# Performance work log

Hardware: AMD Instinct MI355X
Metric: run time of the kernel (lower is better)

## Reference

```python
import jax, jax.numpy as jnp
import numpy as np

H = 2048       # hidden_size
NH = 16        # num query heads
NKV = 4        # num key/value heads
HD = 128       # head_dim
EPS = 1e-6
ROPE_BASE = 10000.0


def rms_norm(x, w):
    xf = x.astype(jnp.float32)
    var = jnp.mean(xf * xf, axis=-1, keepdims=True)
    return (w * (xf * jax.lax.rsqrt(var + EPS)).astype(x.dtype))


def rope_cos_sin(seq_len, dtype):
    inv_freq = 1.0 / (ROPE_BASE ** (jnp.arange(0, HD, 2, dtype=jnp.float32) / HD))
    pos = jnp.arange(seq_len, dtype=jnp.float32)
    ang = pos[:, None] * inv_freq[None, :]            # [S, HD/2]
    emb = jnp.concatenate([ang, ang], axis=-1)        # [S, HD]
    return jnp.cos(emb).astype(dtype), jnp.sin(emb).astype(dtype)


def rotate_half(x):
    x1, x2 = jnp.split(x, 2, axis=-1)
    return jnp.concatenate([-x2, x1], axis=-1)


def setup_inputs() -> dict:
    key = jax.random.key(0)
    ks = jax.random.split(key, 8)
    B, S = 2, 2048
    hidden_states = jax.random.normal(ks[0], (B, S, H), dtype=jnp.float32)
    # additive causal mask [B,1,S,S]
    causal = jnp.where(jnp.tril(jnp.ones((S, S), dtype=bool)), 0.0, -1e9).astype(jnp.float32)
    attention_mask = jnp.broadcast_to(causal[None, None], (B, 1, S, S))
    sc = 1.0 / np.sqrt(H)
    Wq = jax.random.normal(ks[1], (NH * HD, H), dtype=jnp.float32) * sc
    Wk = jax.random.normal(ks[2], (NKV * HD, H), dtype=jnp.float32) * sc
    Wv = jax.random.normal(ks[3], (NKV * HD, H), dtype=jnp.float32) * sc
    Wo = jax.random.normal(ks[4], (H, NH * HD), dtype=jnp.float32) * sc
    q_norm_w = jnp.ones((HD,), dtype=jnp.float32)
    k_norm_w = jnp.ones((HD,), dtype=jnp.float32)
    return {"hidden_states": hidden_states, "attention_mask": attention_mask,
            "Wq": Wq, "Wk": Wk, "Wv": Wv, "Wo": Wo,
            "q_norm_w": q_norm_w, "k_norm_w": k_norm_w}


def reference(hidden_states, attention_mask, Wq, Wk, Wv, Wo, q_norm_w, k_norm_w):
    B, S, _ = hidden_states.shape
    # projections (nn.Linear: x @ W.T)
    q = (hidden_states @ Wq.T).reshape(B, S, NH, HD).transpose(0, 2, 1, 3)   # [B,NH,S,HD]
    k = (hidden_states @ Wk.T).reshape(B, S, NKV, HD).transpose(0, 2, 1, 3)  # [B,NKV,S,HD]
    v = (hidden_states @ Wv.T).reshape(B, S, NKV, HD).transpose(0, 2, 1, 3)
    # QK RMSNorm over head_dim
    q = rms_norm(q, q_norm_w)
    k = rms_norm(k, k_norm_w)
    # RoPE
    cos, sin = rope_cos_sin(S, q.dtype)        # [S,HD]
    q = q * cos + rotate_half(q) * sin
    k = k * cos + rotate_half(k) * sin
    # GQA: repeat kv heads
    n_rep = NH // NKV
    k = jnp.repeat(k, n_rep, axis=1)           # [B,NH,S,HD]
    v = jnp.repeat(v, n_rep, axis=1)
    # attention
    scores = jnp.einsum('bhqd,bhkd->bhqk', q, k) / np.sqrt(HD)
    scores = scores + attention_mask
    probs = jax.nn.softmax(scores, axis=-1)
    attn = jnp.einsum('bhqk,bhkd->bhqd', probs, v)
    attn = attn.transpose(0, 2, 1, 3).reshape(B, S, NH * HD)
    return attn @ Wo.T
```

## Files before the change

### kernel.cpp

```cpp
#include <hip/hip_runtime.h>
#include <hip/hip_bf16.h>
#include <math.h>

#define NH 16
#define NKV 4
#define HD 128
#define SEQ 2048
#define BATCH 2
#define EPSF 1e-6f
#define QKV 3072

typedef __attribute__((ext_vector_type(8))) short bf16x8;
typedef __attribute__((ext_vector_type(4))) short short4v;
typedef __attribute__((ext_vector_type(4))) float f32x4;

__device__ __forceinline__ short f2bf(float x) {
    unsigned u = __float_as_uint(x);
    u += 0x7fffu + ((u >> 16) & 1u);
    return (short)(u >> 16);
}
__device__ __forceinline__ float bf2f(short x) {
    return __uint_as_float((unsigned)(unsigned short)x << 16);
}
__device__ __forceinline__ unsigned pkbf(float a, float b) {
    __hip_bfloat162 h = __float22bfloat162_rn(float2{a, b});
    unsigned r; __builtin_memcpy(&r, &h, 4); return r;
}

__device__ __forceinline__ void gll16(const short* g, short* l) {
    __builtin_amdgcn_global_load_lds(
        (const __attribute__((address_space(1))) unsigned*)g,
        (__attribute__((address_space(3))) unsigned*)l, 16, 0, 0);
}

__global__ __launch_bounds__(256)
void cast_all(const float* __restrict__ hs, const float* __restrict__ Wq,
              const float* __restrict__ Wk, const float* __restrict__ Wv,
              const float* __restrict__ Wo, short* __restrict__ hsb,
              short* __restrict__ wqkv, short* __restrict__ wob)
{
    const size_t MEG = 1024 * 1024;
    const int id = blockIdx.x;
    const float* s;
    short* d;
    size_t off;
    if (id < 8192)       { s = hs; d = hsb;            off = (size_t)id * 1024; }
    else if (id < 12288) { s = Wq; d = wqkv;           off = (size_t)(id - 8192) * 1024; }
    else if (id < 13312) { s = Wk; d = wqkv + 4 * MEG; off = (size_t)(id - 12288) * 1024; }
    else if (id < 14336) { s = Wv; d = wqkv + 5 * MEG; off = (size_t)(id - 13312) * 1024; }
    else                 { s = Wo; d = wob;            off = (size_t)(id - 14336) * 1024; }
    const size_t i = off + threadIdx.x * 4;
    float4 v = *(const float4*)(s + i);
    short4v o;
    o.x = f2bf(v.x); o.y = f2bf(v.y); o.z = f2bf(v.z); o.w = f2bf(v.w);
    *(short4v*)(d + i) = o;
}

template<bool OUT_BF16>
__global__ __launch_bounds__(256, 3)
void gemm_nt_mfma(const short* __restrict__ A, const short* __restrict__ B,
                  void* __restrict__ Cv, int N, int K, int gridX, int total)
{
    __shared__ short As[128 * 64];
    __shared__ short Bs[128 * 64];

    const int tid = threadIdx.x;
    const int w = tid >> 6, lane = tid & 63;
    const int quad = lane >> 4, ln = lane & 15;
    const int mw = (w >> 1) * 64, nw = (w & 1) * 64;

    const int id = blockIdx.x;
    const int t = (id & 7) * (total >> 3) + (id >> 3);
    const int n0 = (t % gridX) * 128;
    const int m0 = (t / gridX) * 128;

    const int rr = lane >> 3;
    const int gsw = ((lane & 7) ^ rr) * 8;
    const short* Ag[4]; const short* Bg[4];
    short* Al[4]; short* Bl[4];
    #pragma unroll
    for (int r = 0; r < 4; ++r) {
        const int row = w * 8 + 32 * r + rr;
        Ag[r] = A + (size_t)(m0 + row) * K + gsw;
        Bg[r] = B + (size_t)(n0 + row) * K + gsw;
        Al[r] = &As[(w * 8 + 32 * r) * 64];
        Bl[r] = &Bs[(w * 8 + 32 * r) * 64];
    }

    const int col0 = ((quad) ^ (ln & 7)) * 8;
    const int col1 = ((4 + quad) ^ (ln & 7)) * 8;

    f32x4 acc[4][4];
    #pragma unroll
    for (int i = 0; i < 4; ++i)
        #pragma unroll
        for (int j = 0; j < 4; ++j)
            acc[i][j] = (f32x4){0.f, 0.f, 0.f, 0.f};

    for (int k0 = 0; k0 < K; k0 += 64) {
        __syncthreads();
        #pragma unroll
        for (int r = 0; r < 4; ++r) {
            gll16(Ag[r] + k0, Al[r]);
            gll16(Bg[r] + k0, Bl[r]);
        }
        __syncthreads();

        #pragma unroll
        for (int ks = 0; ks < 2; ++ks) {
            const int col = ks ? col1 : col0;
            bf16x8 af[4], bfr[4];
            #pragma unroll
            for (int i = 0; i < 4; ++i)
                af[i] = *(const bf16x8*)&As[(mw + i * 16 + ln) * 64 + col];
            #pragma unroll
            for (int j = 0; j < 4; ++j)
                bfr[j] = *(const bf16x8*)&Bs[(nw + j * 16 + ln) * 64 + col];
            #pragma unroll
            for (int i = 0; i < 4; ++i)
                #pragma unroll
                for (int j = 0; j < 4; ++j)
                    acc[i][j] = __builtin_amdgcn_mfma_f32_16x16x32_bf16(
                        af[i], bfr[j], acc[i][j], 0, 0, 0);
        }
    }

    #pragma unroll
    for (int i = 0; i < 4; ++i) {
        #pragma unroll
        for (int reg = 0; reg < 4; ++reg) {
            const int row = m0 + mw + i * 16 + quad * 4 + reg;
            const size_t base = (size_t)row * N + n0 + nw;
            #pragma unroll
            for (int j = 0; j < 4; ++j) {
                if (OUT_BF16)
                    ((short*)Cv)[base + j * 16 + ln] = f2bf(acc[i][j][reg]);
                else
                    ((float*)Cv)[base + j * 16 + ln] = acc[i][j][reg];
            }
        }
    }
}

__global__ __launch_bounds__(256)
void norm_rope_bf16(short* __restrict__ qkv, const float* __restrict__ qw,
                    const float* __restrict__ kw)
{
    const int wave = threadIdx.x >> 6;
    const int lane = threadIdx.x & 63;
    const long vec = (long)blockIdx.x * 4 + wave;
    const long NQ = (long)BATCH * SEQ * NH;

    short* base;
    const float* w;
    int s;
    if (vec < NQ) {
        const long token = vec / NH;
        const int h = (int)(vec % NH);
        s = (int)(token % SEQ);
        base = qkv + token * QKV + h * HD;
        w = qw;
    } else {
        const long t = vec - NQ;
        const long token = t / NKV;
        const int kvh = (int)(t % NKV);
        s = (int)(token % SEQ);
        base = qkv + token * QKV + 2048 + kvh * HD;
        w = kw;
    }

    float x0 = bf2f(base[lane]);
    float x1 = bf2f(base[lane + 64]);
    float ss = x0 * x0 + x1 * x1;
    #pragma unroll
    for (int off = 32; off; off >>= 1) ss += __shfl_xor(ss, off, 64);
    const float r = rsqrtf(ss * (1.0f / HD) + EPSF);
    x0 = x0 * r * w[lane];
    x1 = x1 * r * w[lane + 64];

    const float inv_freq = expf(-(float)lane * (logf(10000.0f) / 64.0f));
    const float ang = (float)s * inv_freq;
    const float c = cosf(ang);
    const float sn = sinf(ang);
    base[lane]      = f2bf(x0 * c - x1 * sn);
    base[lane + 64] = f2bf(x1 * c + x0 * sn);
}

__global__ __launch_bounds__(256)
void transpose_v(const short* __restrict__ qkv, short* __restrict__ vT)
{
    __shared__ short T[32][33];
    const int bx = blockIdx.x;
    const int st = bx & 63;
    const int dt = (bx >> 6) & 3;
    const int bk = bx >> 8;
    const int s0 = st * 32, d0 = dt * 32;
    const int tid = threadIdx.x;
    const long tok0 = (long)(bk >> 2) * SEQ + s0;
    const int kvh = bk & 3;

    const int rs = tid >> 3;
    const int rc = (tid & 7) * 4;
    short4v val = *(const short4v*)(qkv + (tok0 + rs) * QKV + 2560 + kvh * HD + d0 + rc);
    T[rc + 0][rs] = val.x; T[rc + 1][rs] = val.y;
    T[rc + 2][rs] = val.z; T[rc + 3][rs] = val.w;
    __syncthreads();

    const int wd = tid >> 3;
    const int wsc = (tid & 7) * 4;
    short4v ov;
    ov.x = T[wd][wsc + 0]; ov.y = T[wd][wsc + 1];
    ov.z = T[wd][wsc + 2]; ov.w = T[wd][wsc + 3];
    *(short4v*)(vT + ((size_t)bk * HD + d0 + wd) * SEQ + s0 + wsc) = ov;
}

__global__ __launch_bounds__(512, 4)
void flash_attn_mfma(const short* __restrict__ qkv, const short* __restrict__ vT,
                     short* __restrict__ o)
{
    __shared__ short Ks[64][144];
    __shared__ short Vt[128][80];
    __shared__ short Ps[8][16][80];

    const int tid = threadIdx.x;
    const int w = tid >> 6;
    const int lane = tid & 63;
    const int quad = lane >> 4;
    const int ln = lane & 15;
    const int side = w >> 2;
    const int sw = w & 3;

    const int bx = blockIdx.x;
    const int pair = bx & 15;
    const int bh = bx >> 4;
    const int h = bh & 15;
    const int b = bh >> 4;
    const int kvh = h >> 2;
    const int qa = pair, qb = 31 - pair;
    const int qX = side ? qb : qa;
    const int rX = qX * 64 + sw * 16;

    const float SC = 0.08838834764831845f * 1.4426950408889634f;

    bf16x8 qf[4];
    {
        const short* qrow = qkv + (size_t)(b * SEQ + rX + ln) * QKV + h * HD;
        #pragma unroll
        for (int f = 0; f < 4; ++f)
            qf[f] = *(const bf16x8*)(qrow + f * 32 + quad * 8);
    }

    f32x4 Oa[8];
    #pragma unroll
    for (int dg = 0; dg < 8; ++dg) Oa[dg] = (f32x4){0.f, 0.f, 0.f, 0.f};
    float mX = -1e30f, lX = 0.f;

    const short* kbase = qkv + (size_t)(b * SEQ) * QKV + 2048 + kvh * HD;
    const short* vbase = vT + (size_t)(b * NKV + kvh) * HD * SEQ;

    bf16x8 kp[2], vp[2];
    auto prefetch = [&](int k0) {
        #pragma unroll
        for (int i = 0; i < 2; ++i) {
            const int e = tid + i * 512;
            kp[i] = *(const bf16x8*)(kbase + (size_t)(k0 + (e >> 4)) * QKV + (e & 15) * 8);
            vp[i] = *(const bf16x8*)(vbase + (size_t)(e >> 3) * SEQ + k0 + (e & 7) * 8);
        }
    };
    prefetch(0);

    for (int kt = 0; kt <= qb; ++kt) {
        const int k0 = kt * 64;
        __syncthreads();
        #pragma unroll
        for (int i = 0; i < 2; ++i) {
            const int e = tid + i * 512;
            *(bf16x8*)&Ks[e >> 4][(e & 15) * 8] = kp[i];
            *(bf16x8*)&Vt[e >> 3][(e & 7) * 8] = vp[i];
        }
        __syncthreads();
        if (kt < qb) prefetch(k0 + 64);

        if (kt <= qX) {
            f32x4 s[4];
            #pragma unroll
            for (int g = 0; g < 4; ++g) {
                f32x4 acc = (f32x4){0.f, 0.f, 0.f, 0.f};
                #pragma unroll
                for (int f = 0; f < 4; ++f) {
                    bf16x8 kf = *(const bf16x8*)&Ks[g * 16 + ln][f * 32 + quad * 8];
                    acc = __builtin_amdgcn_mfma_f32_16x16x32_bf16(kf, qf[f], acc, 0, 0, 0);
                }
                s[g] = acc;
            }
            if (kt == qX) {
                const int qrow = rX + ln;
                #pragma unroll
                for (int g = 0; g < 4; ++g)
                    #pragma unroll
                    for (int reg = 0; reg < 4; ++reg) {
                        const int key = k0 + g * 16 + quad * 4 + reg;
                        if (key > qrow) s[g][reg] = -1e30f;
                    }
            }
            float mt = s[0][0];
            #pragma unroll
            for (int g = 0; g < 4; ++g)
                #pragma unroll
                for (int reg = 0; reg < 4; ++reg)
                    mt = fmaxf(mt, s[g][reg]);
            mt = fmaxf(mt, __shfl_xor(mt, 16, 64));
            mt = fmaxf(mt, __shfl_xor(mt, 32, 64));
            const float mnew = fmaxf(mX, mt);
            const float c1 = SC * mnew;
            const float alpha = exp2f(__builtin_fmaf(SC, mX, -c1));
            float ps = 0.f;
            #pragma unroll
            for (int g = 0; g < 4; ++g) {
                float p0 = exp2f(__builtin_fmaf(s[g][0], SC, -c1));
                float p1 = exp2f(__builtin_fmaf(s[g][1], SC, -c1));
                float p2 = exp2f(__builtin_fmaf(s[g][2], SC, -c1));
                float p3 = exp2f(__builtin_fmaf(s[g][3], SC, -c1));
                ps += (p0 + p1) + (p2 + p3);
                uint2 pk;
                pk.x = pkbf(p0, p1);
                pk.y = pkbf(p2, p3);
                *(uint2*)&Ps[w][ln][g * 16 + quad * 4] = pk;
            }
            ps += __shfl_xor(ps, 16, 64);
            ps += __shfl_xor(ps, 32, 64);
            lX = lX * alpha + ps;
            mX = mnew;
            #pragma unroll
            for (int dg = 0; dg < 8; ++dg) {
                Oa[dg][0] *= alpha; Oa[dg][1] *= alpha;
                Oa[dg][2] *= alpha; Oa[dg][3] *= alpha;
            }
            __asm volatile("s_waitcnt lgkmcnt(0)" ::: "memory");
            bf16x8 pf0 = *(const bf16x8*)&Ps[w][ln][quad * 8];
            bf16x8 pf1 = *(const bf16x8*)&Ps[w][ln][32 + quad * 8];
            #pragma unroll
            for (int dg = 0; dg < 8; ++dg) {
                bf16x8 vf0 = *(const bf16x8*)&Vt[dg * 16 + ln][quad * 8];
                bf16x8 vf1 = *(const bf16x8*)&Vt[dg * 16 + ln][32 + quad * 8];
                Oa[dg] = __builtin_amdgcn_mfma_f32_16x16x32_bf16(vf0, pf0, Oa[dg], 0, 0, 0);
                Oa[dg] = __builtin_amdgcn_mfma_f32_16x16x32_bf16(vf1, pf1, Oa[dg], 0, 0, 0);
            }
        }
    }

    {
        const float inv = 1.0f / lX;
        short* orow = o + ((size_t)(b * SEQ + rX + ln) * NH + h) * HD;
        #pragma unroll
        for (int dg = 0; dg < 8; ++dg) {
            uint2 ov;
            ov.x = pkbf(Oa[dg][0] * inv, Oa[dg][1] * inv);
            ov.y = pkbf(Oa[dg][2] * inv, Oa[dg][3] * inv);
            *(uint2*)(orow + dg * 16 + quad * 4) = ov;
        }
    }
}

extern "C" void kernel_launch(void* const* d_in, const int* in_sizes, int n_in,
                              void* d_out, int out_size, void* d_ws, size_t ws_size,
                              hipStream_t stream)
{
    const float* hs = (const float*)d_in[0];
    const float* Wq = (const float*)d_in[2];
    const float* Wk = (const float*)d_in[3];
    const float* Wv = (const float*)d_in[4];
    const float* Wo = (const float*)d_in[5];
    const float* qw = (const float*)d_in[6];
    const float* kw = (const float*)d_in[7];
    float* out = (float*)d_out;

    const size_t MEG = 1024 * 1024;
    short* hsb  = (short*)d_ws;
    short* wqkv = hsb + 8 * MEG;
    short* wob  = wqkv + 6 * MEG;
    short* qkvb = wob + 4 * MEG;
    short* vT   = (short*)d_out;

    dim3 blk(256);

    cast_all<<<dim3(18432), blk, 0, stream>>>(hs, Wq, Wk, Wv, Wo, hsb, wqkv, wob);

    gemm_nt_mfma<true><<<dim3(768), blk, 0, stream>>>(
        hsb, wqkv, qkvb, QKV, 2048, 24, 768);

    norm_rope_bf16<<<dim3((BATCH * SEQ * (NH + NKV)) / 4), blk, 0, stream>>>(
        qkvb, qw, kw);

    transpose_v<<<dim3(2048), blk, 0, stream>>>(qkvb, vT);

    flash_attn_mfma<<<dim3(512), dim3(512), 0, stream>>>(qkvb, vT, hsb);

    gemm_nt_mfma<false><<<dim3(512), blk, 0, stream>>>(
        hsb, wob, out, 2048, 2048, 16, 512);
}
```

Measured before the change: 334.3 us.

## Swizzle attention LDS tiles, defer softmax rescale, raise MFMA priority

Replaces the padded LDS arrays for K, V-transposed and P with unpadded tiles using an XOR swizzle on 8-element column groups, which removes bank conflicts and shrinks shared memory. It adds an FA4-style lazy rescale: when the running max grows by at most a threshold, the old max is kept and the alpha rescale of the O accumulators and the row sum is skipped. It also raises wave priority around the MFMA loops with s_setprio. The deferred rescale lets unnormalised exponentials reach up to 2^6 before bf16 packing, which slightly changes numerics.

```diff
diff --git a/kernel.cpp b/kernel.cpp
--- a/kernel.cpp
+++ b/kernel.cpp
@@ -218,15 +218,16 @@
 void flash_attn_mfma(const short* __restrict__ qkv, const short* __restrict__ vT,
                      short* __restrict__ o)
 {
-    __shared__ short Ks[64][144];
-    __shared__ short Vt[128][80];
-    __shared__ short Ps[8][16][80];
+    __shared__ short Ks[64 * 128];
+    __shared__ short Vt[128 * 64];
+    __shared__ short Ps[8][16 * 64];
 
     const int tid = threadIdx.x;
     const int w = tid >> 6;
     const int lane = tid & 63;
     const int quad = lane >> 4;
     const int ln = lane & 15;
+    const int lnm = ln & 7;
     const int side = w >> 2;
     const int sw = w & 3;
 
@@ -242,6 +243,15 @@
 
     const float SC = 0.08838834764831845f * 1.4426950408889634f;
 
+    int colK[4];
+    #pragma unroll
+    for (int f = 0; f < 4; ++f) {
+        const int lg = f * 4 + quad;
+        colK[f] = ((lg & 8) | ((lg ^ lnm) & 7)) * 8;
+    }
+    const int colA = (quad ^ lnm) * 8;
+    const int colB = ((4 + quad) ^ lnm) * 8;
+
     bf16x8 qf[4];
     {
         const short* qrow = qkv + (size_t)(b * SEQ + rX + ln) * QKV + h * HD;
@@ -275,24 +285,28 @@
         #pragma unroll
         for (int i = 0; i < 2; ++i) {
             const int e = tid + i * 512;
-            *(bf16x8*)&Ks[e >> 4][(e & 15) * 8] = kp[i];
-            *(bf16x8*)&Vt[e >> 3][(e & 7) * 8] = vp[i];
+            const int kr = e >> 4, kg = e & 15;
+            *(bf16x8*)&Ks[kr * 128 + ((kg & 8) | ((kg ^ (kr & 7)) & 7)) * 8] = kp[i];
+            const int vd = e >> 3, vg = e & 7;
+            *(bf16x8*)&Vt[vd * 64 + ((vg ^ (vd & 7)) * 8)] = vp[i];
         }
         __syncthreads();
         if (kt < qb) prefetch(k0 + 64);
 
         if (kt <= qX) {
             f32x4 s[4];
+            __builtin_amdgcn_s_setprio(1);
             #pragma unroll
             for (int g = 0; g < 4; ++g) {
                 f32x4 acc = (f32x4){0.f, 0.f, 0.f, 0.f};
                 #pragma unroll
                 for (int f = 0; f < 4; ++f) {
-                    bf16x8 kf = *(const bf16x8*)&Ks[g * 16 + ln][f * 32 + quad * 8];
+                    bf16x8 kf = *(const bf16x8*)&Ks[(g * 16 + ln) * 128 + colK[f]];
                     acc = __builtin_amdgcn_mfma_f32_16x16x32_bf16(kf, qf[f], acc, 0, 0, 0);
                 }
                 s[g] = acc;
             }
+            __builtin_amdgcn_s_setprio(0);
             if (kt == qX) {
                 const int qrow = rX + ln;
                 #pragma unroll
@@ -312,7 +326,9 @@
             mt = fmaxf(mt, __shfl_xor(mt, 16, 64));
             mt = fmaxf(mt, __shfl_xor(mt, 32, 64));
             const float mnew = fmaxf(mX, mt);
-            const float c1 = SC * mnew;
+            const bool defer = __all((mnew - mX) * SC <= 6.0f);
+            const float mref = defer ? mX : mnew;
+            const float c1 = SC * mref;
             const float alpha = exp2f(__builtin_fmaf(SC, mX, -c1));
             float ps = 0.f;
             #pragma unroll
@@ -325,27 +341,34 @@
                 uint2 pk;
                 pk.x = pkbf(p0, p1);
                 pk.y = pkbf(p2, p3);
-                *(uint2*)&Ps[w][ln][g * 16 + quad * 4] = pk;
+                const int sg = (2 * g + (quad >> 1)) ^ lnm;
+                *(uint2*)&Ps[w][ln * 64 + sg * 8 + (quad & 1) * 4] = pk;
             }
             ps += __shfl_xor(ps, 16, 64);
             ps += __shfl_xor(ps, 32, 64);
-            lX = lX * alpha + ps;
-            mX = mnew;
+            mX = mref;
+            if (defer) {
+                lX += ps;
+            } else {
+                lX = lX * alpha + ps;
+                #pragma unroll
+                for (int dg = 0; dg < 8; ++dg) {
+                    Oa[dg][0] *= alpha; Oa[dg][1] *= alpha;
+                    Oa[dg][2] *= alpha; Oa[dg][3] *= alpha;
+                }
+            }
+            __asm volatile("s_waitcnt lgkmcnt(0)" ::: "memory");
+            bf16x8 pf0 = *(const bf16x8*)&Ps[w][ln * 64 + colA];
+            bf16x8 pf1 = *(const bf16x8*)&Ps[w][ln * 64 + colB];
+            __builtin_amdgcn_s_setprio(1);
             #pragma unroll
             for (int dg = 0; dg < 8; ++dg) {
-                Oa[dg][0] *= alpha; Oa[dg][1] *= alpha;
-                Oa[dg][2] *= alpha; Oa[dg][3] *= alpha;
-            }
-            __asm volatile("s_waitcnt lgkmcnt(0)" ::: "memory");
-            bf16x8 pf0 = *(const bf16x8*)&Ps[w][ln][quad * 8];
-            bf16x8 pf1 = *(const bf16x8*)&Ps[w][ln][32 + quad * 8];
-            #pragma unroll
-            for (int dg = 0; dg < 8; ++dg) {
-                bf16x8 vf0 = *(const bf16x8*)&Vt[dg * 16 + ln][quad * 8];
-                bf16x8 vf1 = *(const bf16x8*)&Vt[dg * 16 + ln][32 + quad * 8];
+                bf16x8 vf0 = *(const bf16x8*)&Vt[(dg * 16 + ln) * 64 + colA];
+                bf16x8 vf1 = *(const bf16x8*)&Vt[(dg * 16 + ln) * 64 + colB];
                 Oa[dg] = __builtin_amdgcn_mfma_f32_16x16x32_bf16(vf0, pf0, Oa[dg], 0, 0, 0);
                 Oa[dg] = __builtin_amdgcn_mfma_f32_16x16x32_bf16(vf1, pf1, Oa[dg], 0, 0, 0);
             }
+            __builtin_amdgcn_s_setprio(0);
         }
     }
 
```

Result: faster. 327.1 us (-2.1%).
